# Optimization experiments

Measured on AMD Instinct MI355X. Metric: run time of the kernel, lower is better.

## Reference

```python
import jax, jax.numpy as jnp
import numpy as np

B, T, I, H, D = 4, 4096, 1024, 16, 64


def setup_inputs() -> dict:
    key = jax.random.key(0)
    k1, k2, k3 = jax.random.split(key, 3)
    inputs = jax.random.normal(k1, (B, T, I), dtype=jnp.float32)
    kv_kernel = jax.random.normal(k2, (I, H, D, 2), dtype=jnp.float32) * (1.0 / np.sqrt(I))
    q_kernel = jax.random.normal(k3, (H, D), dtype=jnp.float32) * (1.0 / np.sqrt(D))
    return {"inputs": inputs, "kv_kernel": kv_kernel, "q_kernel": q_kernel}


def _combine(a, b):
    # state layout along last axis: [m (1), u (1), w (D)]
    ma, ua, wa = a[..., :1], a[..., 1:2], a[..., 2:]
    mb, ub, wb = b[..., :1], b[..., 1:2], b[..., 2:]
    m = jnp.maximum(ma, mb)
    ea = jnp.exp(ma - m)
    eb = jnp.exp(mb - m)
    return jnp.concatenate([m, ua * ea + ub * eb, wa * ea + wb * eb], axis=-1)


def reference(inputs, kv_kernel, q_kernel):
    # inputs: (B,T,I); kv_kernel: (I,H,D,2); q_kernel: (H,D)
    kv = jnp.einsum('bti,ihdk->bthdk', inputs, kv_kernel)
    kv = jax.nn.silu(kv)
    k = kv[..., 0]  # (B,T,H,D)
    v = kv[..., 1]  # (B,T,H,D)
    st = jnp.einsum('hd,bthd->bth', q_kernel, k)[..., None]  # (B,T,H,1)
    u_init = jnp.ones_like(st)
    elems = jnp.concatenate([st, u_init, v], axis=-1)  # (B,T,H,2+D)
    o = jax.lax.associative_scan(_combine, elems, axis=1)
    c = o[..., 1:2]  # denominator (B,T,H,1)
    a = o[..., 2:]   # numerator   (B,T,H,D)
    h = a / c        # (B,T,H,D)
    # concat_heads=False -> mean over heads
    return jnp.mean(h, axis=-2)  # (B,T,D)
```

## Files before the change

### kernel.cpp

```cpp
#include <hip/hip_runtime.h>
#include <hip/hip_bf16.h>
#include <math.h>

constexpr int B_ = 4, T_ = 4096, I_ = 1024, H_ = 16, D_ = 64;
constexpr int M_ = B_ * T_;
constexpr int N_ = H_ * D_ * 2;
constexpr int C_ = 64;
constexpr int L_ = T_ / C_;
constexpr int NT_ = 16;

typedef __bf16 bf16x8 __attribute__((ext_vector_type(8)));
typedef float  f32x4  __attribute__((ext_vector_type(4)));

__device__ __forceinline__ float silu_f(float x) {
    return x / (1.0f + __expf(-x));
}

__device__ __forceinline__ ushort f2bf_u(float x) {
    unsigned u = __float_as_uint(x);
    unsigned r = (u + 0x7fffu + ((u >> 16) & 1u)) >> 16;
    return (ushort)r;
}
__device__ __forceinline__ float bfu2f(ushort u) {
    return __uint_as_float(((unsigned)u) << 16);
}

__device__ __forceinline__ void gload_lds16(const void* g, void* l) {
    __builtin_amdgcn_global_load_lds(
        (const __attribute__((address_space(1))) unsigned int*)g,
        (__attribute__((address_space(3))) unsigned int*)l, 16, 0, 0);
}

__global__ __launch_bounds__(256) void convert_fused_kernel(
    const float* __restrict__ A,  ushort* __restrict__ A2,
    const float* __restrict__ Bm, ushort* __restrict__ B2T)
{
    __shared__ float tile[64][65];
    const int tid = threadIdx.x;
    if (blockIdx.x < 16384) {
        int idx = blockIdx.x * 256 + tid;
        int m  = idx >> 8;
        int kq = (idx & 255) * 4;
        float4 a = *reinterpret_cast<const float4*>(&A[(size_t)m * 1024 + kq]);
        ushort4 hi;
        hi.x = f2bf_u(a.x);
        hi.y = f2bf_u(a.y);
        hi.z = f2bf_u(a.z);
        hi.w = f2bf_u(a.w);
        *reinterpret_cast<ushort4*>(&A2[(size_t)m * 1024 + kq]) = hi;
    } else {
        int bk = blockIdx.x - 16384;
        const int k0 = (bk & 15) * 64;
        const int n0 = (bk >> 4) * 64;
        #pragma unroll
        for (int p = 0; p < 4; ++p) {
            int f = tid + p * 256;
            int r  = f >> 4;
            int c4 = (f & 15) * 4;
            float4 v = *reinterpret_cast<const float4*>(
                &Bm[(size_t)(k0 + r) * 2048 + n0 + c4]);
            tile[r][c4 + 0] = v.x; tile[r][c4 + 1] = v.y;
            tile[r][c4 + 2] = v.z; tile[r][c4 + 3] = v.w;
        }
        __syncthreads();
        #pragma unroll
        for (int p = 0; p < 4; ++p) {
            int f = tid + p * 256;
            int n  = f >> 4;
            int kq = (f & 15) * 4;
            ushort4 hi;
            hi.x = f2bf_u(tile[kq + 0][n]);
            hi.y = f2bf_u(tile[kq + 1][n]);
            hi.z = f2bf_u(tile[kq + 2][n]);
            hi.w = f2bf_u(tile[kq + 3][n]);
            *reinterpret_cast<ushort4*>(&B2T[(size_t)(n0 + n) * 1024 + k0 + kq]) = hi;
        }
    }
}

__device__ __forceinline__ int akof(int t) { return t * 64; }
__device__ __forceinline__ int bkof(int t) { return t * 64; }

#define BARRIER do { asm volatile("" ::: "memory"); \
    __builtin_amdgcn_s_barrier(); \
    asm volatile("" ::: "memory"); } while (0)
#define WAITLGKM asm volatile("s_waitcnt lgkmcnt(0)" ::: "memory")
#define WAITVM(n) asm volatile("s_waitcnt vmcnt(" #n ")" ::: "memory")

#define STAGE(gptr, kb, ldsoff, rs2) do { \
    gload_lds16((gptr) + (kb),         lds + (ldsoff) + tid * 8); \
    gload_lds16((gptr) + (kb) + (rs2), lds + (ldsoff) + 4096 + tid * 8); \
} while (0)

#define RDA(ab, i, kk) (*reinterpret_cast<const bf16x8*>((ab) + (i) * 1024 + ((kk) ? ck1 : ck0)))
#define RDB(bb, j, kk) (*reinterpret_cast<const bf16x8*>((bb) + (j) * 1024 + ((kk) ? ck1 : ck0)))

#define PH_READ_A(ab, ibase) do { \
    _Pragma("unroll") for (int i_ = 0; i_ < 4; ++i_) { \
        a[i_][0] = RDA(ab, (ibase) + i_, 0); \
        a[i_][1] = RDA(ab, (ibase) + i_, 1); } } while (0)
#define PH_READ_B(bb, breg, jbase) do { \
    _Pragma("unroll") for (int j_ = 0; j_ < 2; ++j_) { \
        breg[j_][0] = RDB(bb, (jbase) + j_, 0); \
        breg[j_][1] = RDB(bb, (jbase) + j_, 1); } } while (0)

#define QUAD(IH, BREG, JB) do { \
    __builtin_amdgcn_s_setprio(1); \
    _Pragma("unroll") for (int i_ = 0; i_ < 4; ++i_) \
    _Pragma("unroll") for (int j_ = 0; j_ < 2; ++j_) \
    _Pragma("unroll") for (int k_ = 0; k_ < 2; ++k_) \
        acc[(IH) + i_][(JB) + j_] = __builtin_amdgcn_mfma_f32_16x16x32_bf16( \
            a[i_][k_], BREG[j_][k_], acc[(IH) + i_][(JB) + j_], 0, 0, 0); \
    __builtin_amdgcn_s_setprio(0); \
} while (0)

__global__ __launch_bounds__(512, 2) void gemm_mfma8_kernel(
    const ushort* __restrict__ A2,
    const ushort* __restrict__ B2T,
    const float* __restrict__ qk,
    ushort* __restrict__ v_buf,
    float* __restrict__ s_buf,
    float* __restrict__ agg_m,
    float* __restrict__ agg_u,
    float* __restrict__ agg_w)
{
    __shared__ ushort lds[65536];
    __shared__ float spart[8][128];
    __shared__ float s_lds[2][256];

    const int bid = blockIdx.x;
    const int swz = (bid & 7) * 64 + (bid >> 3);
    const int bx  = swz >> 6;
    const int by  = swz & 63;
    const int m0  = by * 256;
    const int n0  = bx * 256;

    const int tid  = threadIdx.x;
    const int lane = tid & 63;
    const int wid  = tid >> 6;
    const int wr = wid >> 2, wc = wid & 3;
    const int l15 = lane & 15, lg = lane >> 4;

    const int row0 = tid >> 3;
    const int ch0  = (tid & 7) ^ (row0 & 7);
    const ushort* pA  = A2  + (size_t)(m0 + row0) * 1024 + ch0 * 8;
    const ushort* pB  = B2T + (size_t)(n0 + row0) * 1024 + ch0 * 8;
    const ushort* pA1 = pA + 128 * 1024;
    const ushort* pB1 = pB + 128 * 1024;

    const int ck0 = ((0 + lg) ^ (l15 & 7)) * 8;
    const int ck1 = ((4 + lg) ^ (l15 & 7)) * 8;
    const ushort* aB0 = lds + (wr * 128 + l15) * 64;
    const ushort* bB0 = lds + 16384 + (wc * 64 + l15) * 64;
    const ushort* aB1 = aB0 + 32768;
    const ushort* bB1 = bB0 + 32768;

    f32x4 acc[8][4];
    #pragma unroll
    for (int i = 0; i < 8; ++i)
        #pragma unroll
        for (int j = 0; j < 4; ++j)
            acc[i][j] = (f32x4){0.f, 0.f, 0.f, 0.f};
    bf16x8 a[4][2], b01[2][2], b23[2][2];

    {
        STAGE(pA,  akof(0), 0,             65536);
        STAGE(pA1, akof(0), 8192,          65536);
        STAGE(pB,  bkof(0), 16384,         65536);
        STAGE(pB1, bkof(0), 16384 + 8192,  65536);
        STAGE(pB,  bkof(1), 49152,         65536);
        STAGE(pA,  akof(1), 32768,         65536);
        WAITVM(4);
        BARRIER;
    }

    #pragma unroll 1
    for (int I = 0; I < NT_ / 2 - 1; ++I) {
        const int t1g = 2 * I + 1, t2g = 2 * I + 2, t3g = 2 * I + 3;
        const int ak1 = akof(t1g), bk1 = bkof(t1g);
        const int ak2 = akof(t2g), bk2 = bkof(t2g);
        const int ak3 = akof(t3g), bk3 = bkof(t3g);
        PH_READ_A(aB0, 0); PH_READ_B(bB0, b01, 0);
        STAGE(pA1, ak1, 32768 + 8192, 65536);
        BARRIER; WAITLGKM; QUAD(0, b01, 0); BARRIER;
        PH_READ_B(bB0, b23, 2);
        STAGE(pB1, bk1, 49152 + 8192, 65536);
        BARRIER; WAITLGKM; QUAD(0, b23, 2); BARRIER;
        PH_READ_A(aB0, 4);
        STAGE(pB, bk2, 16384, 65536);
        BARRIER; WAITLGKM; QUAD(4, b01, 0); BARRIER;
        STAGE(pA, ak2, 0, 65536);
        WAITVM(4);
        BARRIER; QUAD(4, b23, 2); BARRIER;
        PH_READ_A(aB1, 0); PH_READ_B(bB1, b01, 0);
        STAGE(pA1, ak2, 8192, 65536);
        BARRIER; WAITLGKM; QUAD(0, b01, 0); BARRIER;
        PH_READ_B(bB1, b23, 2);
        STAGE(pB1, bk2, 16384 + 8192, 65536);
        BARRIER; WAITLGKM; QUAD(0, b23, 2); BARRIER;
        PH_READ_A(aB1, 4);
        STAGE(pB, bk3, 49152, 65536);
        BARRIER; WAITLGKM; QUAD(4, b01, 0); BARRIER;
        STAGE(pA, ak3, 32768, 65536);
        WAITVM(4);
        BARRIER; QUAD(4, b23, 2); BARRIER;
    }

    {
        const int t1g = NT_ - 1;
        const int ak1 = akof(t1g), bk1 = bkof(t1g);
        PH_READ_A(aB0, 0); PH_READ_B(bB0, b01, 0);
        STAGE(pA1, ak1, 32768 + 8192, 65536);
        BARRIER; WAITLGKM; QUAD(0, b01, 0); BARRIER;
        PH_READ_B(bB0, b23, 2);
        STAGE(pB1, bk1, 49152 + 8192, 65536);
        BARRIER; WAITLGKM; QUAD(0, b23, 2); BARRIER;
        PH_READ_A(aB0, 4);
        BARRIER; WAITLGKM; QUAD(4, b01, 0); BARRIER;
        WAITVM(0);
        BARRIER; QUAD(4, b23, 2); BARRIER;
        PH_READ_A(aB1, 0); PH_READ_B(bB1, b01, 0);
        BARRIER; WAITLGKM; QUAD(0, b01, 0); BARRIER;
        PH_READ_B(bB1, b23, 2);
        BARRIER; WAITLGKM; QUAD(0, b23, 2); BARRIER;
        PH_READ_A(aB1, 4);
        BARRIER; WAITLGKM; QUAD(4, b01, 0); BARRIER;
        QUAD(4, b23, 2);
    }

    const int hloc  = wc >> 1;
    const int h     = 2 * bx + hloc;
    const int dbase = (wc & 1) * 32 + (l15 >> 1);
    float qv[4];
    #pragma unroll
    for (int j = 0; j < 4; ++j) qv[j] = qk[h * 64 + dbase + j * 8];
    const bool kcol = ((l15 & 1) == 0);

    #pragma unroll
    for (int i = 0; i < 8; ++i) {
        #pragma unroll
        for (int rr = 0; rr < 4; ++rr) {
            int rloc = wr * 128 + i * 16 + lg * 4 + rr;
            int m = m0 + rloc;
            int b = m >> 12, tt = m & 4095;
            float p = 0.f;
            #pragma unroll
            for (int j = 0; j < 4; ++j) {
                float sv = silu_f(acc[i][j][rr]);
                if (kcol) {
                    p += qv[j] * sv;
                } else {
                    v_buf[((size_t)(b * H_ + h) * T_ + tt) * D_ + dbase + j * 8] =
                        f2bf_u(sv);
                }
            }
            p += __shfl_xor(p, 2);
            p += __shfl_xor(p, 4);
            p += __shfl_xor(p, 8);
            if (l15 == 0) spart[wid][i * 16 + lg * 4 + rr] = p;
        }
    }
    __syncthreads();
    {
        int wr2 = tid >> 8, hl = (tid >> 7) & 1, row = tid & 127;
        int m = m0 + wr2 * 128 + row;
        int b = m >> 12, tt = m & 4095;
        float sval = spart[wr2 * 4 + hl * 2][row] + spart[wr2 * 4 + hl * 2 + 1][row];
        s_buf[(size_t)(b * H_ + 2 * bx + hl) * T_ + tt] = sval;
        s_lds[hl][wr2 * 128 + row] = sval;
    }
    __syncthreads();

    {
        const int b  = m0 >> 12;
        #pragma unroll
        for (int cc = 0; cc < 2; ++cc) {
            const int c_l = wr * 2 + cc;
            const int cg  = ((m0 & 4095) >> 6) + c_l;
            float mm = -INFINITY, u = 0.f;
            float w0 = 0.f, w1 = 0.f, w2 = 0.f, w3 = 0.f;
            #pragma unroll
            for (int ir = 0; ir < 4; ++ir) {
                #pragma unroll
                for (int rr = 0; rr < 4; ++rr) {
                    float s  = s_lds[hloc][c_l * 64 + ir * 16 + lg * 4 + rr];
                    float mn = fmaxf(mm, s);
                    float ea = __expf(mm - mn);
                    float eb = __expf(s - mn);
                    u  = u * ea + eb;
                    w0 = w0 * ea + silu_f(acc[cc * 4 + ir][0][rr]) * eb;
                    w1 = w1 * ea + silu_f(acc[cc * 4 + ir][1][rr]) * eb;
                    w2 = w2 * ea + silu_f(acc[cc * 4 + ir][2][rr]) * eb;
                    w3 = w3 * ea + silu_f(acc[cc * 4 + ir][3][rr]) * eb;
                    mm = mn;
                }
            }
            #pragma unroll
            for (int mk = 16; mk <= 32; mk <<= 1) {
                float om = __shfl_xor(mm, mk);
                float ou = __shfl_xor(u,  mk);
                float o0 = __shfl_xor(w0, mk);
                float o1 = __shfl_xor(w1, mk);
                float o2 = __shfl_xor(w2, mk);
                float o3 = __shfl_xor(w3, mk);
                float mn = fmaxf(mm, om);
                float ea = __expf(mm - mn);
                float eb = __expf(om - mn);
                u  = u * ea + ou * eb;
                w0 = w0 * ea + o0 * eb;
                w1 = w1 * ea + o1 * eb;
                w2 = w2 * ea + o2 * eb;
                w3 = w3 * ea + o3 * eb;
                mm = mn;
            }
            const int base = (b * H_ + h) * C_ + cg;
            if ((wc & 1) == 0 && lane == 0) {
                agg_m[base] = mm;
                agg_u[base] = u;
            }
            if (!kcol && lg == 0) {
                agg_w[(size_t)base * D_ + dbase + 0 ] = w0;
                agg_w[(size_t)base * D_ + dbase + 8 ] = w1;
                agg_w[(size_t)base * D_ + dbase + 16] = w2;
                agg_w[(size_t)base * D_ + dbase + 24] = w3;
            }
        }
    }
}

#define TILE_M 128
#define TILE_N 128
#define TILE_K 16
__global__ __launch_bounds__(256) void gemm_kv_kernel(
    const float* __restrict__ A, const float* __restrict__ Bm,
    const float* __restrict__ q, ushort* __restrict__ v_buf,
    float* __restrict__ s_buf)
{
    __shared__ float As[TILE_K][TILE_M + 4];
    __shared__ float Bs[TILE_K][TILE_N + 4];
    const int tid = threadIdx.x;
    const int h   = blockIdx.x;
    const int bm  = blockIdx.y;
    const int m0  = bm * TILE_M;
    const int n0  = h * TILE_N;
    const int tx = tid & 15, ty = tid >> 4;
    float acc[8][8];
    #pragma unroll
    for (int i = 0; i < 8; ++i)
        #pragma unroll
        for (int j = 0; j < 8; ++j) acc[i][j] = 0.f;
    for (int k0 = 0; k0 < I_; k0 += TILE_K) {
        #pragma unroll
        for (int p = 0; p < 2; ++p) {
            int f = tid + p * 256;
            int row = f >> 2, kq = (f & 3) * 4;
            float4 av = *reinterpret_cast<const float4*>(
                &A[(size_t)(m0 + row) * I_ + k0 + kq]);
            As[kq + 0][row] = av.x; As[kq + 1][row] = av.y;
            As[kq + 2][row] = av.z; As[kq + 3][row] = av.w;
        }
        #pragma unroll
        for (int p = 0; p < 2; ++p) {
            int f = tid + p * 256;
            int row = f >> 5, c4 = (f & 31) * 4;
            *reinterpret_cast<float4*>(&Bs[row][c4]) =
                *reinterpret_cast<const float4*>(
                    &Bm[(size_t)(k0 + row) * N_ + n0 + c4]);
        }
        __syncthreads();
        #pragma unroll
        for (int kk = 0; kk < TILE_K; ++kk) {
            float4 a0 = *reinterpret_cast<const float4*>(&As[kk][ty * 8]);
            float4 a1 = *reinterpret_cast<const float4*>(&As[kk][ty * 8 + 4]);
            float4 b0 = *reinterpret_cast<const float4*>(&Bs[kk][tx * 8]);
            float4 b1 = *reinterpret_cast<const float4*>(&Bs[kk][tx * 8 + 4]);
            float af[8] = {a0.x, a0.y, a0.z, a0.w, a1.x, a1.y, a1.z, a1.w};
            float bf[8] = {b0.x, b0.y, b0.z, b0.w, b1.x, b1.y, b1.z, b1.w};
            #pragma unroll
            for (int i = 0; i < 8; ++i)
                #pragma unroll
                for (int j = 0; j < 8; ++j)
                    acc[i][j] = fmaf(af[i], bf[j], acc[i][j]);
        }
        __syncthreads();
    }
    float4 qv = *reinterpret_cast<const float4*>(&q[h * D_ + tx * 4]);
    float qf[4] = {qv.x, qv.y, qv.z, qv.w};
    #pragma unroll
    for (int i = 0; i < 8; ++i) {
        int m = m0 + ty * 8 + i;
        int b = m >> 12, t = m & 4095;
        float partial = 0.f;
        #pragma unroll
        for (int j = 0; j < 4; ++j) {
            float kval = silu_f(acc[i][2 * j]);
            float vv = silu_f(acc[i][2 * j + 1]);
            v_buf[((size_t)(b * H_ + h) * T_ + t) * D_ + tx * 4 + j] = f2bf_u(vv);
            partial = fmaf(qf[j], kval, partial);
        }
        #pragma unroll
        for (int mask = 8; mask >= 1; mask >>= 1)
            partial += __shfl_xor(partial, mask, 16);
        if (tx == 0) s_buf[(size_t)(b * H_ + h) * T_ + t] = partial;
    }
}

__global__ __launch_bounds__(64) void chunk_agg_kernel(
    const float* __restrict__ s_buf, const ushort* __restrict__ v_buf,
    float* __restrict__ agg_m, float* __restrict__ agg_u,
    float* __restrict__ agg_w)
{
    const int x    = blockIdx.x;
    const int c    = x & (C_ - 1);
    const int bh   = x >> 6;
    const int lane = threadIdx.x;
    const float* sp  = s_buf + (size_t)bh * T_ + c * L_;
    const ushort* vp = v_buf + ((size_t)bh * T_ + c * L_) * D_ + lane;
    float m = -INFINITY, u = 0.f, w = 0.f;
    for (int t = 0; t < L_; ++t) {
        float s  = sp[t];
        float vv = bfu2f(vp[(size_t)t * D_]);
        float mn = fmaxf(m, s);
        float ea = __expf(m - mn);
        float eb = __expf(s - mn);
        u = u * ea + eb;
        w = w * ea + vv * eb;
        m = mn;
    }
    if (lane == 0) { agg_m[x] = m; agg_u[x] = u; }
    agg_w[(size_t)x * D_ + lane] = w;
}

__global__ __launch_bounds__(64) void chunk_prefix_kernel(
    float* __restrict__ agg_m, float* __restrict__ agg_u,
    float* __restrict__ agg_w)
{
    const int bh   = blockIdx.x;
    const int lane = threadIdx.x;
    float pm = -INFINITY, pu = 0.f, pw = 0.f;
    #pragma unroll 4
    for (int c = 0; c < C_; ++c) {
        int base = bh * C_ + c;
        float am = agg_m[base];
        float au = agg_u[base];
        float aw = agg_w[(size_t)base * D_ + lane];
        if (lane == 0) { agg_m[base] = pm; agg_u[base] = pu; }
        agg_w[(size_t)base * D_ + lane] = pw;
        float mn = fmaxf(pm, am);
        float ea = __expf(pm - mn);
        float eb = __expf(am - mn);
        pu = pu * ea + au * eb;
        pw = pw * ea + aw * eb;
        pm = mn;
    }
}

__global__ __launch_bounds__(256) void scan_apply_kernel(
    const float* __restrict__ s_buf, const ushort* __restrict__ v_buf,
    const float* __restrict__ agg_m, const float* __restrict__ agg_u,
    const float* __restrict__ agg_w, float* __restrict__ out)
{
    __shared__ float part[4][8][64];
    const int bx   = blockIdx.x;
    const int b    = bx >> 6;
    const int c    = bx & (C_ - 1);
    const int w    = threadIdx.x >> 6;
    const int lane = threadIdx.x & 63;
    float m[4], u[4], ws[4];
    #pragma unroll
    for (int j = 0; j < 4; ++j) {
        int h = w * 4 + j;
        int base = (b * H_ + h) * C_ + c;
        m[j]  = agg_m[base];
        u[j]  = agg_u[base];
        ws[j] = agg_w[(size_t)base * D_ + lane];
    }
    const int t0 = c * L_;
    for (int g = 0; g < L_ / 8; ++g) {
        #pragma unroll
        for (int qq = 0; qq < 8; ++qq) {
            int t = t0 + g * 8 + qq;
            float acc = 0.f;
            #pragma unroll
            for (int j = 0; j < 4; ++j) {
                int h = w * 4 + j;
                size_t bht = (size_t)(b * H_ + h) * T_ + t;
                float s  = s_buf[bht];
                float vv = bfu2f(v_buf[bht * D_ + lane]);
                float mn = fmaxf(m[j], s);
                float ea = __expf(m[j] - mn);
                float eb = __expf(s - mn);
                u[j]  = u[j] * ea + eb;
                ws[j] = ws[j] * ea + vv * eb;
                m[j]  = mn;
                acc += ws[j] / u[j];
            }
            part[w][qq][lane] = acc;
        }
        __syncthreads();
        {
            int e  = threadIdx.x;
            int tt = e >> 6, d = e & 63;
            float sum = part[0][tt][d] + part[1][tt][d]
                      + part[2][tt][d] + part[3][tt][d];
            out[((size_t)b * T_ + (t0 + g * 8 + tt)) * D_ + d] = sum * (1.f / 16.f);
        }
        {
            int e  = threadIdx.x + 256;
            int tt = e >> 6, d = e & 63;
            float sum = part[0][tt][d] + part[1][tt][d]
                      + part[2][tt][d] + part[3][tt][d];
            out[((size_t)b * T_ + (t0 + g * 8 + tt)) * D_ + d] = sum * (1.f / 16.f);
        }
        __syncthreads();
    }
}

extern "C" void kernel_launch(void* const* d_in, const int* in_sizes, int n_in,
                              void* d_out, int out_size, void* d_ws, size_t ws_size,
                              hipStream_t stream) {
    const float* A  = (const float*)d_in[0];
    const float* Bm = (const float*)d_in[1];
    const float* q  = (const float*)d_in[2];
    float* out = (float*)d_out;

    ushort* v_buf = (ushort*)d_ws;
    float*  s_buf = (float*)(v_buf + (size_t)B_ * H_ * T_ * D_);
    float*  agg_m = s_buf + (size_t)B_ * H_ * T_;
    float*  agg_u = agg_m + B_ * H_ * C_;
    float*  agg_w = agg_u + B_ * H_ * C_;
    ushort* A2    = (ushort*)(agg_w + (size_t)B_ * H_ * C_ * D_);
    ushort* B2T   = A2 + (size_t)M_ * 1024;

    size_t need = (size_t)B_ * H_ * T_ * D_ * 2
                + ((size_t)262144 + 4096 + 4096 + 262144) * 4
                + ((size_t)M_ * 1024 + (size_t)2048 * 1024) * 2;

    if (ws_size >= need) {
        convert_fused_kernel<<<16896, 256, 0, stream>>>(A, A2, Bm, B2T);
        gemm_mfma8_kernel<<<512, 512, 0, stream>>>(A2, B2T, q, v_buf, s_buf,
                                                   agg_m, agg_u, agg_w);
    } else {
        dim3 ggrid(H_, M_ / TILE_M);
        gemm_kv_kernel<<<ggrid, 256, 0, stream>>>(A, Bm, q, v_buf, s_buf);
        chunk_agg_kernel<<<B_ * H_ * C_, 64, 0, stream>>>(s_buf, v_buf,
                                                          agg_m, agg_u, agg_w);
    }
    chunk_prefix_kernel<<<B_ * H_, 64, 0, stream>>>(agg_m, agg_u, agg_w);
    scan_apply_kernel<<<B_ * C_, 256, 0, stream>>>(s_buf, v_buf, agg_m, agg_u, agg_w, out);
}
```

Baseline: 153.5 us.

## Merge GEMM main-loop phases to halve barriers and regroup tile staging

Restructures the GEMM main loop from eight barrier-separated phases per iteration into four. Each phase now reads both B fragment halves and issues two QUADs of MFMAs. The global-to-LDS staging is reordered so each phase stages both halves of one A or B tile, and the prologue now prefetches the second B half instead of the next A tile. This removes half the workgroup barriers and gives longer MFMA runs, but it raises register pressure by keeping more fragments live and changes the prefetch distance, which may expose memory latency.

```diff
diff --git a/kernel.cpp b/kernel.cpp
--- a/kernel.cpp
+++ b/kernel.cpp
@@ -169,7 +169,7 @@
         STAGE(pB,  bkof(0), 16384,         65536);
         STAGE(pB1, bkof(0), 16384 + 8192,  65536);
         STAGE(pB,  bkof(1), 49152,         65536);
-        STAGE(pA,  akof(1), 32768,         65536);
+        STAGE(pB1, bkof(1), 49152 + 8192,  65536);
         WAITVM(4);
         BARRIER;
     }
@@ -177,55 +177,57 @@
     #pragma unroll 1
     for (int I = 0; I < NT_ / 2 - 1; ++I) {
         const int t1g = 2 * I + 1, t2g = 2 * I + 2, t3g = 2 * I + 3;
-        const int ak1 = akof(t1g), bk1 = bkof(t1g);
+        const int ak1 = akof(t1g);
         const int ak2 = akof(t2g), bk2 = bkof(t2g);
-        const int ak3 = akof(t3g), bk3 = bkof(t3g);
-        PH_READ_A(aB0, 0); PH_READ_B(bB0, b01, 0);
+        const int bk3 = bkof(t3g);
+        PH_READ_A(aB0, 0); PH_READ_B(bB0, b01, 0); PH_READ_B(bB0, b23, 2);
+        STAGE(pA,  ak1, 32768,        65536);
         STAGE(pA1, ak1, 32768 + 8192, 65536);
-        BARRIER; WAITLGKM; QUAD(0, b01, 0); BARRIER;
-        PH_READ_B(bB0, b23, 2);
-        STAGE(pB1, bk1, 49152 + 8192, 65536);
-        BARRIER; WAITLGKM; QUAD(0, b23, 2); BARRIER;
+        BARRIER; WAITLGKM;
+        QUAD(0, b01, 0); QUAD(0, b23, 2);
+        BARRIER;
         PH_READ_A(aB0, 4);
-        STAGE(pB, bk2, 16384, 65536);
-        BARRIER; WAITLGKM; QUAD(4, b01, 0); BARRIER;
-        STAGE(pA, ak2, 0, 65536);
+        STAGE(pB,  bk2, 16384,         65536);
+        STAGE(pB1, bk2, 16384 + 8192,  65536);
         WAITVM(4);
-        BARRIER; QUAD(4, b23, 2); BARRIER;
-        PH_READ_A(aB1, 0); PH_READ_B(bB1, b01, 0);
+        BARRIER; WAITLGKM;
+        QUAD(4, b01, 0); QUAD(4, b23, 2);
+        BARRIER;
+        PH_READ_A(aB1, 0); PH_READ_B(bB1, b01, 0); PH_READ_B(bB1, b23, 2);
+        STAGE(pA,  ak2, 0,    65536);
         STAGE(pA1, ak2, 8192, 65536);
-        BARRIER; WAITLGKM; QUAD(0, b01, 0); BARRIER;
-        PH_READ_B(bB1, b23, 2);
-        STAGE(pB1, bk2, 16384 + 8192, 65536);
-        BARRIER; WAITLGKM; QUAD(0, b23, 2); BARRIER;
+        BARRIER; WAITLGKM;
+        QUAD(0, b01, 0); QUAD(0, b23, 2);
+        BARRIER;
         PH_READ_A(aB1, 4);
-        STAGE(pB, bk3, 49152, 65536);
-        BARRIER; WAITLGKM; QUAD(4, b01, 0); BARRIER;
-        STAGE(pA, ak3, 32768, 65536);
+        STAGE(pB,  bk3, 49152,         65536);
+        STAGE(pB1, bk3, 49152 + 8192,  65536);
         WAITVM(4);
-        BARRIER; QUAD(4, b23, 2); BARRIER;
+        BARRIER; WAITLGKM;
+        QUAD(4, b01, 0); QUAD(4, b23, 2);
+        BARRIER;
     }
 
     {
-        const int t1g = NT_ - 1;
-        const int ak1 = akof(t1g), bk1 = bkof(t1g);
-        PH_READ_A(aB0, 0); PH_READ_B(bB0, b01, 0);
+        const int ak1 = akof(NT_ - 1);
+        PH_READ_A(aB0, 0); PH_READ_B(bB0, b01, 0); PH_READ_B(bB0, b23, 2);
+        STAGE(pA,  ak1, 32768,        65536);
         STAGE(pA1, ak1, 32768 + 8192, 65536);
-        BARRIER; WAITLGKM; QUAD(0, b01, 0); BARRIER;
-        PH_READ_B(bB0, b23, 2);
-        STAGE(pB1, bk1, 49152 + 8192, 65536);
-        BARRIER; WAITLGKM; QUAD(0, b23, 2); BARRIER;
+        BARRIER; WAITLGKM;
+        QUAD(0, b01, 0); QUAD(0, b23, 2);
+        BARRIER;
         PH_READ_A(aB0, 4);
-        BARRIER; WAITLGKM; QUAD(4, b01, 0); BARRIER;
         WAITVM(0);
-        BARRIER; QUAD(4, b23, 2); BARRIER;
-        PH_READ_A(aB1, 0); PH_READ_B(bB1, b01, 0);
-        BARRIER; WAITLGKM; QUAD(0, b01, 0); BARRIER;
-        PH_READ_B(bB1, b23, 2);
-        BARRIER; WAITLGKM; QUAD(0, b23, 2); BARRIER;
+        BARRIER; WAITLGKM;
+        QUAD(4, b01, 0); QUAD(4, b23, 2);
+        BARRIER;
+        PH_READ_A(aB1, 0); PH_READ_B(bB1, b01, 0); PH_READ_B(bB1, b23, 2);
+        BARRIER; WAITLGKM;
+        QUAD(0, b01, 0); QUAD(0, b23, 2);
+        BARRIER;
         PH_READ_A(aB1, 4);
-        BARRIER; WAITLGKM; QUAD(4, b01, 0); BARRIER;
-        QUAD(4, b23, 2);
+        BARRIER; WAITLGKM;
+        QUAD(4, b01, 0); QUAD(4, b23, 2);
     }
 
     const int hloc  = wc >> 1;
```

Result: no change. 156.4 us (+1.9%).
